# Optimization experiments

Measured on AMD Instinct MI355X. Metric: run time of the kernel, lower is better.

Reference implementation:

```python
import jax, jax.numpy as jnp
import numpy as np

GRID_SIZE = 25
DAMPING = 0.01


def setup_inputs() -> dict:
    key = jax.random.key(0)
    k1, k2 = jax.random.split(key)
    local_x = jax.random.normal(k1, (1, 4, 1000, 1000), dtype=jnp.float32)
    ms_history = jax.random.normal(k2, (1, 16, 4, 1000, 1000), dtype=jnp.float32)
    return {"local_x": local_x, "ms_history": ms_history}


def _project(local_x, ms_history):
    new_hist = ms_history[0]                      # (nt, nb, nx, ny)
    nt, nb, nx, ny = new_hist.shape
    nb2 = local_x.shape[1]
    ngs = GRID_SIZE
    ngx, ngy = nx // ngs, ny // ngs
    K, P = nb * nt, ngs * ngs
    # tile-ize: (ngx, ngy, K, P) and (ngx, ngy, nb2, P)
    V = new_hist.reshape(K, ngx, ngs, ngy, ngs).transpose(1, 3, 0, 2, 4).reshape(ngx, ngy, K, P)
    X = local_x.reshape(nb2, ngx, ngs, ngy, ngs).transpose(1, 3, 0, 2, 4).reshape(ngx, ngy, nb2, P)
    # batched damped Gram matrix: (ngx, ngy, K, K)
    G = jnp.einsum('xykp,xylp->xykl', V, V) + DAMPING * jnp.eye(K, dtype=V.dtype)
    Ginv = jnp.linalg.inv(G)                      # batched small inverse
    A = jnp.einsum('xycp,xykp->xyck', X, V)       # X @ V^T : (ngx, ngy, nb2, K)
    AG = jnp.einsum('xyck,xykl->xycl', A, Ginv)   # X @ V^T @ inv(G)
    Y = jnp.einsum('xycl,xylp->xycp', AG, V)      # projected tiles: (ngx, ngy, nb2, P)
    # re-assemble spatial image: (1, nb2, nx, ny)
    W = Y.reshape(ngx, ngy, nb2, ngs, ngs).transpose(2, 0, 3, 1, 4).reshape(1, nb2, nx, ny)
    return W


def reference(local_x, ms_history):
    return _project(local_x, ms_history)
```

## Files before the change

### kernel.cpp

```cpp
#include <hip/hip_runtime.h>

#define NGS 25
#define NGX 40
#define NGY 40
#define KK  64
#define NB2 4
#define NYY 1000
#define PTOT 625
#define PC  128
#define NCH 5
#define DAMP 0.01f

typedef __attribute__((ext_vector_type(8))) short short8;
typedef __attribute__((ext_vector_type(4))) float f32x4;

__device__ __forceinline__ short bf16_rn(float x) {
  unsigned u = __float_as_uint(x);
  u = u + 0x7fffu + ((u >> 16) & 1u);
  return (short)(u >> 16);
}
__device__ __forceinline__ float bf16_tof(short s) {
  return __uint_as_float(((unsigned)(unsigned short)s) << 16);
}

__global__ __launch_bounds__(256, 4) void k_gram_solve(
    const float* __restrict__ xin, const float* __restrict__ hist,
    float* __restrict__ AG)
{
  __shared__ __align__(16) short smem[2 * 80 * 128];
  short* Vhi = smem;
  short* Vlo = smem + 80 * 128;
  float (*Gs)[KK + 5] = (float (*)[KK + 5])smem;
  float* prow = ((float*)smem) + 4416;

  const int tile = blockIdx.x;
  const int gx = tile / NGY, gy = tile % NGY;
  const size_t base = (size_t)(gx * NGS) * NYY + (size_t)(gy * NGS);
  const int tid  = threadIdx.x;
  const int wave = tid >> 6;
  const int lane = tid & 63;
  const int u    = lane >> 4;
  const int col  = lane & 15;

  const int pp = tid & 127;
  const int rb = tid >> 7;

  for (int i = tid + 68 * 128; i < 80 * 128; i += 256) { Vhi[i] = 0; Vlo[i] = 0; }

  f32x4 accG[4];
  #pragma unroll
  for (int j = 0; j < 4; ++j) { accG[j].x = 0.f; accG[j].y = 0.f; accG[j].z = 0.f; accG[j].w = 0.f; }
  f32x4 accX; accX.x = 0.f; accX.y = 0.f; accX.z = 0.f; accX.w = 0.f;

  const int rA = 16 * wave + col;
  const int rX = KK + col;

  #define STW(r, val) { \
    const short h = (short)(__float_as_uint(val) >> 16); \
    const short l = bf16_rn((val) - bf16_tof(h)); \
    const int off = (r) * 128 + ((((pp >> 3) ^ ((r) & 7)) << 3) | (pp & 7)); \
    Vhi[off] = h; Vlo[off] = l; }

  for (int ch = 0; ch < NCH; ++ch) {
    const int p = ch * PC + pp;
    const bool inb = (p < PTOT);
    const int px = p / NGS, py = p - px * NGS;
    const size_t a = base + (size_t)px * NYY + py;

    float v0[12], v1[12], v2[10];
    #pragma unroll
    for (int it = 0; it < 12; ++it)
      v0[it] = inb ? hist[(size_t)(rb + 2 * it) * 1000000 + a] : 0.f;
    #pragma unroll
    for (int it = 0; it < 12; ++it)
      v1[it] = inb ? hist[(size_t)(rb + 2 * (it + 12)) * 1000000 + a] : 0.f;
    #pragma unroll
    for (int it = 0; it < 12; ++it) STW(rb + 2 * it, v0[it]);
    #pragma unroll
    for (int it = 0; it < 10; ++it) {
      const int r = rb + 2 * (it + 24);
      v2[it] = inb ? ((it < 8) ? hist[(size_t)r * 1000000 + a]
                               : xin[(size_t)(r - KK) * 1000000 + a]) : 0.f;
    }
    #pragma unroll
    for (int it = 0; it < 12; ++it) STW(rb + 2 * (it + 12), v1[it]);
    #pragma unroll
    for (int it = 0; it < 10; ++it) STW(rb + 2 * (it + 24), v2[it]);
    __syncthreads();

    #pragma unroll
    for (int t = 0; t < 4; ++t) {
      const int k8 = t * 4 + u;
      #define FRG(P, r) (*(const short8*)&P[(r) * 128 + (((k8) ^ ((r) & 7)) << 3)])
      const short8 a_hi = FRG(Vhi, rA);
      const short8 a_lo = FRG(Vlo, rA);
      const short8 x_hi = FRG(Vhi, rX);
      const short8 x_lo = FRG(Vlo, rX);
      short8 b_hi[4], b_lo[4];
      #pragma unroll
      for (int s = 0; s < 4; ++s) {
        b_hi[s] = FRG(Vhi, 16 * s + col);
        b_lo[s] = FRG(Vlo, 16 * s + col);
      }
      #undef FRG
      #pragma unroll
      for (int j = 0; j < 4; ++j) {
        accG[j] = __builtin_amdgcn_mfma_f32_16x16x32_bf16(a_hi, b_hi[j], accG[j], 0, 0, 0);
        accG[j] = __builtin_amdgcn_mfma_f32_16x16x32_bf16(a_hi, b_lo[j], accG[j], 0, 0, 0);
        accG[j] = __builtin_amdgcn_mfma_f32_16x16x32_bf16(a_lo, b_hi[j], accG[j], 0, 0, 0);
      }
      accX = __builtin_amdgcn_mfma_f32_16x16x32_bf16(x_hi, a_hi, accX, 0, 0, 0);
      accX = __builtin_amdgcn_mfma_f32_16x16x32_bf16(x_hi, a_lo, accX, 0, 0, 0);
      accX = __builtin_amdgcn_mfma_f32_16x16x32_bf16(x_lo, a_hi, accX, 0, 0, 0);
    }
    __syncthreads();
  }
  #undef STW

  const int row4 = u * 4;
  #pragma unroll
  for (int j = 0; j < 4; ++j)
    #pragma unroll
    for (int q = 0; q < 4; ++q) {
      const int gr = 16 * wave + row4 + q;
      const int gc = 16 * j + col;
      float g = (q == 0) ? accG[j].x : (q == 1) ? accG[j].y : (q == 2) ? accG[j].z : accG[j].w;
      Gs[gr][gc] = g + ((gr == gc) ? DAMP : 0.f);
    }
  if (lane < 16) {
    Gs[16 * wave + lane][KK + 0] = accX.x;
    Gs[16 * wave + lane][KK + 1] = accX.y;
    Gs[16 * wave + lane][KK + 2] = accX.z;
    Gs[16 * wave + lane][KK + 3] = accX.w;
  }
  __syncthreads();

  const int ei = tid >> 2, eq = tid & 3;
  float v[17];
  #pragma unroll
  for (int jj = 0; jj < 17; ++jj) v[jj] = Gs[ei][4 * jj + eq];

  float myDiag = 1.f;
  if (ei == 0) {
    #pragma unroll
    for (int jj = 0; jj < 17; ++jj) prow[4 * jj + eq] = v[jj];
  }
  __syncthreads();

  #pragma unroll
  for (int k = 0; k < KK; ++k) {
    const float* pr = prow + (k & 1) * 72;
    const float piv = pr[k];
    const float num = __shfl(v[k >> 2], (lane & ~3) | (k & 3), 64);
    const float f = (ei == k) ? 0.f : (num / piv);
    if (ei == k) myDiag = piv;
    #pragma unroll
    for (int jj = (k < 3 ? 0 : (k - 2) >> 2); jj < 17; ++jj)
      v[jj] -= f * pr[4 * jj + eq];
    if (k < KK - 1) {
      if (ei == k + 1) {
        float* pw = prow + ((k + 1) & 1) * 72;
        #pragma unroll
        for (int jj = 0; jj < 17; ++jj) pw[4 * jj + eq] = v[jj];
      }
    }
    __syncthreads();
  }

  AG[(size_t)tile * 256 + eq * 64 + ei] = v[16] / myDiag;
}

__global__ __launch_bounds__(256) void k_project(
    const float* __restrict__ hist, const float* __restrict__ AG,
    float* __restrict__ out)
{
  __shared__ float ag[KK][NB2];
  const int tile = blockIdx.x;
  const int gx = tile / NGY, gy = tile % NGY;
  const size_t base = (size_t)(gx * NGS) * NYY + (size_t)(gy * NGS);
  const int tid = threadIdx.x;
  {
    const int c = tid >> 6, k = tid & 63;
    ag[k][c] = AG[(size_t)tile * 256 + tid];
  }
  __syncthreads();

  const int p1 = tid, p2 = tid + 256, p3 = tid + 512;
  const int a1 = (p1 / NGS) * NYY + (p1 % NGS);
  const int a2 = (p2 / NGS) * NYY + (p2 % NGS);
  const bool has3 = (p3 < PTOT);
  const int a3 = has3 ? ((p3 / NGS) * NYY + (p3 % NGS)) : 0;

  float o1[4] = {0,0,0,0}, o2[4] = {0,0,0,0}, o3[4] = {0,0,0,0};
  const float4* ag4 = (const float4*)ag;

  #pragma unroll 4
  for (int k = 0; k < KK; ++k) {
    const size_t ko = (size_t)k * 1000000 + base;
    const float v1 = hist[ko + a1];
    const float v2 = hist[ko + a2];
    const float v3 = has3 ? hist[ko + a3] : 0.f;
    const float4 w = ag4[k];
    o1[0] += w.x * v1; o1[1] += w.y * v1; o1[2] += w.z * v1; o1[3] += w.w * v1;
    o2[0] += w.x * v2; o2[1] += w.y * v2; o2[2] += w.z * v2; o2[3] += w.w * v2;
    o3[0] += w.x * v3; o3[1] += w.y * v3; o3[2] += w.z * v3; o3[3] += w.w * v3;
  }

  out[(size_t)0 * 1000000 + base + a1] = o1[0];
  out[(size_t)1 * 1000000 + base + a1] = o1[1];
  out[(size_t)2 * 1000000 + base + a1] = o1[2];
  out[(size_t)3 * 1000000 + base + a1] = o1[3];
  out[(size_t)0 * 1000000 + base + a2] = o2[0];
  out[(size_t)1 * 1000000 + base + a2] = o2[1];
  out[(size_t)2 * 1000000 + base + a2] = o2[2];
  out[(size_t)3 * 1000000 + base + a2] = o2[3];
  if (has3) {
    out[(size_t)0 * 1000000 + base + a3] = o3[0];
    out[(size_t)1 * 1000000 + base + a3] = o3[1];
    out[(size_t)2 * 1000000 + base + a3] = o3[2];
    out[(size_t)3 * 1000000 + base + a3] = o3[3];
  }
}

extern "C" void kernel_launch(void* const* d_in, const int* in_sizes, int n_in,
                              void* d_out, int out_size, void* d_ws, size_t ws_size,
                              hipStream_t stream) {
  const float* xin  = (const float*)d_in[0];
  const float* hist = (const float*)d_in[1];
  float* out = (float*)d_out;
  float* AG  = (float*)d_ws;

  k_gram_solve<<<NGX * NGY, 256, 0, stream>>>(xin, hist, AG);
  k_project  <<<NGX * NGY, 256, 0, stream>>>(hist, AG, out);
}
```

Before: 219.8 us.

## Split Gram accumulation across waves by pixel chunks, exploit symmetry

Each wave now owns independent 32-pixel chunks with a private LDS slice and computes the full 64x64 Gram plus X·V^T for its chunks. Only the upper-triangular blocks are computed, which cuts MFMA work, and the per-chunk block barriers are removed. The four partial results are then reduced serially into shared memory. This adds more accumulator registers and a sequential four-step reduction, and the occupancy hint in launch bounds is dropped.

```diff
diff --git a/kernel.cpp b/kernel.cpp
--- a/kernel.cpp
+++ b/kernel.cpp
@@ -7,8 +7,7 @@
 #define NB2 4
 #define NYY 1000
 #define PTOT 625
-#define PC  128
-#define NCH 5
+#define PC  32
 #define DAMP 0.01f
 
 typedef __attribute__((ext_vector_type(8))) short short8;
@@ -23,15 +22,13 @@
   return __uint_as_float(((unsigned)(unsigned short)s) << 16);
 }
 
-__global__ __launch_bounds__(256, 4) void k_gram_solve(
+__global__ __launch_bounds__(256) void k_gram_solve(
     const float* __restrict__ xin, const float* __restrict__ hist,
     float* __restrict__ AG)
 {
-  __shared__ __align__(16) short smem[2 * 80 * 128];
-  short* Vhi = smem;
-  short* Vlo = smem + 80 * 128;
+  __shared__ __align__(16) short smem[4 * 2 * 80 * PC + 288];
   float (*Gs)[KK + 5] = (float (*)[KK + 5])smem;
-  float* prow = ((float*)smem) + 4416;
+  float* prow = (float*)(smem + 4 * 2 * 80 * PC);
 
   const int tile = blockIdx.x;
   const int gx = tile / NGY, gy = tile % NGY;
@@ -42,108 +39,127 @@
   const int u    = lane >> 4;
   const int col  = lane & 15;
 
-  const int pp = tid & 127;
-  const int rb = tid >> 7;
-
-  for (int i = tid + 68 * 128; i < 80 * 128; i += 256) { Vhi[i] = 0; Vlo[i] = 0; }
-
-  f32x4 accG[4];
-  #pragma unroll
-  for (int j = 0; j < 4; ++j) { accG[j].x = 0.f; accG[j].y = 0.f; accG[j].z = 0.f; accG[j].w = 0.f; }
-  f32x4 accX; accX.x = 0.f; accX.y = 0.f; accX.z = 0.f; accX.w = 0.f;
-
-  const int rA = 16 * wave + col;
-  const int rX = KK + col;
+  short* Whi = smem + wave * (2 * 80 * PC);
+  short* Wlo = Whi + 80 * PC;
+
+  for (int i = lane; i < 12 * PC; i += 64) { Whi[68 * PC + i] = 0; Wlo[68 * PC + i] = 0; }
+
+  f32x4 accG[10];
+  f32x4 accA[4];
+  #pragma unroll
+  for (int j = 0; j < 10; ++j) { accG[j].x = 0.f; accG[j].y = 0.f; accG[j].z = 0.f; accG[j].w = 0.f; }
+  #pragma unroll
+  for (int j = 0; j < 4; ++j) { accA[j].x = 0.f; accA[j].y = 0.f; accA[j].z = 0.f; accA[j].w = 0.f; }
+
+  const int pp = lane & 31;
+  const int rh = lane >> 5;
 
   #define STW(r, val) { \
     const short h = (short)(__float_as_uint(val) >> 16); \
     const short l = bf16_rn((val) - bf16_tof(h)); \
-    const int off = (r) * 128 + ((((pp >> 3) ^ ((r) & 7)) << 3) | (pp & 7)); \
-    Vhi[off] = h; Vlo[off] = l; }
-
-  for (int ch = 0; ch < NCH; ++ch) {
+    const int off = (r) * PC + ((((pp >> 3) ^ ((r) & 3)) << 3) | (pp & 7)); \
+    Whi[off] = h; Wlo[off] = l; }
+
+  for (int cw = 0; cw < 5; ++cw) {
+    const int ch = wave + 4 * cw;
     const int p = ch * PC + pp;
     const bool inb = (p < PTOT);
     const int px = p / NGS, py = p - px * NGS;
     const size_t a = base + (size_t)px * NYY + py;
 
-    float v0[12], v1[12], v2[10];
-    #pragma unroll
-    for (int it = 0; it < 12; ++it)
-      v0[it] = inb ? hist[(size_t)(rb + 2 * it) * 1000000 + a] : 0.f;
-    #pragma unroll
-    for (int it = 0; it < 12; ++it)
-      v1[it] = inb ? hist[(size_t)(rb + 2 * (it + 12)) * 1000000 + a] : 0.f;
-    #pragma unroll
-    for (int it = 0; it < 12; ++it) STW(rb + 2 * it, v0[it]);
-    #pragma unroll
-    for (int it = 0; it < 10; ++it) {
-      const int r = rb + 2 * (it + 24);
-      v2[it] = inb ? ((it < 8) ? hist[(size_t)r * 1000000 + a]
+    float v0[17], v1[17];
+    #pragma unroll
+    for (int it = 0; it < 17; ++it)
+      v0[it] = inb ? hist[(size_t)(2 * it + rh) * 1000000 + a] : 0.f;
+    #pragma unroll
+    for (int it = 0; it < 17; ++it) {
+      const int r = 34 + 2 * it + rh;
+      v1[it] = inb ? ((r < KK) ? hist[(size_t)r * 1000000 + a]
                                : xin[(size_t)(r - KK) * 1000000 + a]) : 0.f;
     }
     #pragma unroll
-    for (int it = 0; it < 12; ++it) STW(rb + 2 * (it + 12), v1[it]);
-    #pragma unroll
-    for (int it = 0; it < 10; ++it) STW(rb + 2 * (it + 24), v2[it]);
+    for (int it = 0; it < 17; ++it) STW(2 * it + rh, v0[it]);
+    #pragma unroll
+    for (int it = 0; it < 17; ++it) STW(34 + 2 * it + rh, v1[it]);
+
+    #define FRG(P, r) (*(const short8*)&P[(r) * PC + (((u) ^ ((r) & 3)) << 3)])
+    short8 fh[4], fl[4];
+    #pragma unroll
+    for (int s = 0; s < 4; ++s) { fh[s] = FRG(Whi, 16 * s + col); fl[s] = FRG(Wlo, 16 * s + col); }
+    const short8 xh = FRG(Whi, KK + col);
+    const short8 xl = FRG(Wlo, KK + col);
+    #undef FRG
+
+    #pragma unroll
+    for (int si = 0; si < 4; ++si)
+      #pragma unroll
+      for (int sj = 0; sj < 4; ++sj) {
+        if (sj >= si) {
+          const int ix = si * 4 - (si * (si + 1)) / 2 + sj;
+          accG[ix] = __builtin_amdgcn_mfma_f32_16x16x32_bf16(fh[si], fh[sj], accG[ix], 0, 0, 0);
+          accG[ix] = __builtin_amdgcn_mfma_f32_16x16x32_bf16(fh[si], fl[sj], accG[ix], 0, 0, 0);
+          accG[ix] = __builtin_amdgcn_mfma_f32_16x16x32_bf16(fl[si], fh[sj], accG[ix], 0, 0, 0);
+        }
+      }
+    #pragma unroll
+    for (int s = 0; s < 4; ++s) {
+      accA[s] = __builtin_amdgcn_mfma_f32_16x16x32_bf16(xh, fh[s], accA[s], 0, 0, 0);
+      accA[s] = __builtin_amdgcn_mfma_f32_16x16x32_bf16(xh, fl[s], accA[s], 0, 0, 0);
+      accA[s] = __builtin_amdgcn_mfma_f32_16x16x32_bf16(xl, fh[s], accA[s], 0, 0, 0);
+    }
+  }
+  #undef STW
+
+  __syncthreads();
+  for (int g = 0; g < 4; ++g) {
+    if (wave == g) {
+      #pragma unroll
+      for (int si = 0; si < 4; ++si)
+        #pragma unroll
+        for (int sj = 0; sj < 4; ++sj) {
+          if (sj >= si) {
+            const int ix = si * 4 - (si * (si + 1)) / 2 + sj;
+            #pragma unroll
+            for (int q = 0; q < 4; ++q) {
+              const float val = (q == 0) ? accG[ix].x : (q == 1) ? accG[ix].y
+                              : (q == 2) ? accG[ix].z : accG[ix].w;
+              const int r0 = 16 * si + 4 * u + q;
+              const int c0 = 16 * sj + col;
+              if (g == 0) {
+                Gs[r0][c0] = val + ((r0 == c0) ? DAMP : 0.f);
+                if (si != sj) Gs[c0][r0] = val;
+              } else {
+                Gs[r0][c0] += val;
+                if (si != sj) Gs[c0][r0] += val;
+              }
+            }
+          }
+        }
+      if (lane < 16) {
+        #pragma unroll
+        for (int s = 0; s < 4; ++s) {
+          #pragma unroll
+          for (int q = 0; q < 4; ++q) {
+            const float val = (q == 0) ? accA[s].x : (q == 1) ? accA[s].y
+                            : (q == 2) ? accA[s].z : accA[s].w;
+            if (g == 0) Gs[16 * s + lane][KK + q] = val;
+            else        Gs[16 * s + lane][KK + q] += val;
+          }
+        }
+      }
+    }
     __syncthreads();
-
-    #pragma unroll
-    for (int t = 0; t < 4; ++t) {
-      const int k8 = t * 4 + u;
-      #define FRG(P, r) (*(const short8*)&P[(r) * 128 + (((k8) ^ ((r) & 7)) << 3)])
-      const short8 a_hi = FRG(Vhi, rA);
-      const short8 a_lo = FRG(Vlo, rA);
-      const short8 x_hi = FRG(Vhi, rX);
-      const short8 x_lo = FRG(Vlo, rX);
-      short8 b_hi[4], b_lo[4];
-      #pragma unroll
-      for (int s = 0; s < 4; ++s) {
-        b_hi[s] = FRG(Vhi, 16 * s + col);
-        b_lo[s] = FRG(Vlo, 16 * s + col);
-      }
-      #undef FRG
-      #pragma unroll
-      for (int j = 0; j < 4; ++j) {
-        accG[j] = __builtin_amdgcn_mfma_f32_16x16x32_bf16(a_hi, b_hi[j], accG[j], 0, 0, 0);
-        accG[j] = __builtin_amdgcn_mfma_f32_16x16x32_bf16(a_hi, b_lo[j], accG[j], 0, 0, 0);
-        accG[j] = __builtin_amdgcn_mfma_f32_16x16x32_bf16(a_lo, b_hi[j], accG[j], 0, 0, 0);
-      }
-      accX = __builtin_amdgcn_mfma_f32_16x16x32_bf16(x_hi, a_hi, accX, 0, 0, 0);
-      accX = __builtin_amdgcn_mfma_f32_16x16x32_bf16(x_hi, a_lo, accX, 0, 0, 0);
-      accX = __builtin_amdgcn_mfma_f32_16x16x32_bf16(x_lo, a_hi, accX, 0, 0, 0);
-    }
-    __syncthreads();
-  }
-  #undef STW
-
-  const int row4 = u * 4;
-  #pragma unroll
-  for (int j = 0; j < 4; ++j)
-    #pragma unroll
-    for (int q = 0; q < 4; ++q) {
-      const int gr = 16 * wave + row4 + q;
-      const int gc = 16 * j + col;
-      float g = (q == 0) ? accG[j].x : (q == 1) ? accG[j].y : (q == 2) ? accG[j].z : accG[j].w;
-      Gs[gr][gc] = g + ((gr == gc) ? DAMP : 0.f);
-    }
-  if (lane < 16) {
-    Gs[16 * wave + lane][KK + 0] = accX.x;
-    Gs[16 * wave + lane][KK + 1] = accX.y;
-    Gs[16 * wave + lane][KK + 2] = accX.z;
-    Gs[16 * wave + lane][KK + 3] = accX.w;
-  }
-  __syncthreads();
+  }
 
   const int ei = tid >> 2, eq = tid & 3;
-  float v[17];
-  #pragma unroll
-  for (int jj = 0; jj < 17; ++jj) v[jj] = Gs[ei][4 * jj + eq];
+  float w[17];
+  #pragma unroll
+  for (int jj = 0; jj < 17; ++jj) w[jj] = Gs[ei][4 * jj + eq];
 
   float myDiag = 1.f;
   if (ei == 0) {
     #pragma unroll
-    for (int jj = 0; jj < 17; ++jj) prow[4 * jj + eq] = v[jj];
+    for (int jj = 0; jj < 17; ++jj) prow[4 * jj + eq] = w[jj];
   }
   __syncthreads();
 
@@ -151,23 +167,23 @@
   for (int k = 0; k < KK; ++k) {
     const float* pr = prow + (k & 1) * 72;
     const float piv = pr[k];
-    const float num = __shfl(v[k >> 2], (lane & ~3) | (k & 3), 64);
+    const float num = __shfl(w[k >> 2], (lane & ~3) | (k & 3), 64);
     const float f = (ei == k) ? 0.f : (num / piv);
     if (ei == k) myDiag = piv;
     #pragma unroll
     for (int jj = (k < 3 ? 0 : (k - 2) >> 2); jj < 17; ++jj)
-      v[jj] -= f * pr[4 * jj + eq];
+      w[jj] -= f * pr[4 * jj + eq];
     if (k < KK - 1) {
       if (ei == k + 1) {
         float* pw = prow + ((k + 1) & 1) * 72;
         #pragma unroll
-        for (int jj = 0; jj < 17; ++jj) pw[4 * jj + eq] = v[jj];
+        for (int jj = 0; jj < 17; ++jj) pw[4 * jj + eq] = w[jj];
       }
     }
     __syncthreads();
   }
 
-  AG[(size_t)tile * 256 + eq * 64 + ei] = v[16] / myDiag;
+  AG[(size_t)tile * 256 + eq * 64 + ei] = w[16] / myDiag;
 }
 
 __global__ __launch_bounds__(256) void k_project(
```

Measured after the change: 263.1 us. 1.2x slower.
